# Kernel optimization log

Measured on AMD Instinct MI355X. Metric: run time of the kernel, lower is better.

Reference implementation:

```python
import jax, jax.numpy as jnp
from jax import lax
import numpy as np
import math

IMG_H, IMG_W = 592, 800  # stride-16 image for a 50x37 feature map


def _make_anchors(fx=50, fy=37, base=8, dsr=16):
    rows = []
    for x in range(fx):
        for y in range(fy):
            for size in [base, 2 * base, 4 * base]:
                rows.append([(x - size / 2) * dsr, (y - size / 2) * dsr,
                             (x + size / 2) * dsr, (y + size / 2) * dsr])
                s = math.sqrt(size ** 2 / 2)
                rows.append([(x - s) * dsr, (y - s / 2) * dsr, (x + s) * dsr, (y + s / 2) * dsr])
                rows.append([(x - s / 2) * dsr, (y - s) * dsr, (x + s / 2) * dsr, (y + s) * dsr])
    return np.array(rows, np.float32)


def setup_inputs() -> dict:
    key = jax.random.key(0)
    k = jax.random.split(key, 8)
    B, G, H, W = 32, 20, 50, 37
    feats = jax.random.normal(k[0], (B, 512, H, W), jnp.float32)
    a = _make_anchors()
    keep = (a[:, 0] >= 0) & (a[:, 1] >= 0) & (a[:, 2] <= IMG_W) & (a[:, 3] <= IMG_H)
    idxs_inside = jnp.asarray(np.nonzero(keep)[0].astype(np.int32))
    anchors = jnp.asarray(a[keep])
    # valid xyxy GT boxes inside the image
    x1 = jax.random.uniform(k[1], (B, G)) * (IMG_W - 160)
    y1 = jax.random.uniform(k[2], (B, G)) * (IMG_H - 160)
    w = 32.0 + jax.random.uniform(k[3], (B, G)) * 96.0
    h = 32.0 + jax.random.uniform(k[4], (B, G)) * 96.0
    gt_boxes = jnp.stack([x1, y1, x1 + w, y1 + h], -1)
    W3 = jax.random.normal(k[5], (512, 512, 3, 3), jnp.float32) * 0.02
    b3 = jnp.zeros((512,), jnp.float32)
    Wcls = jax.random.normal(k[6], (18, 512, 1, 1), jnp.float32) * 0.02
    bcls = jnp.zeros((18,), jnp.float32)
    Wloc = jax.random.normal(k[7], (36, 512, 1, 1), jnp.float32) * 0.02
    bloc = jnp.zeros((36,), jnp.float32)
    return {"feats": feats, "gt_boxes": gt_boxes, "anchors": anchors,
            "W3": W3, "b3": b3, "Wcls": Wcls, "bcls": bcls,
            "Wloc": Wloc, "bloc": bloc, "idxs_inside": idxs_inside}


def _conv(x, w, b, pad):
    y = lax.conv_general_dilated(x, w, (1, 1), pad,
                                 dimension_numbers=("NCHW", "OIHW", "NCHW"))
    return y + b[None, :, None, None]


def reference(feats, gt_boxes, anchors, W3, b3, Wcls, bcls, Wloc, bloc, idxs_inside):
    B = feats.shape[0]
    rpn_conv1 = jax.nn.relu(_conv(feats, W3, b3, "SAME"))
    cls_score = _conv(rpn_conv1, Wcls, bcls, "VALID")          # [B,18,H,W]
    _, C, H, Wd = cls_score.shape
    logits = cls_score.reshape(B, 2, (C * H) // 2, Wd)          # reshape(x, 2)
    prob = jax.nn.softmax(logits, axis=1)
    prob_back = prob.reshape(B, C, H, Wd)                       # reshape back to 18
    loc_pred = _conv(rpn_conv1, Wloc, bloc, "VALID")            # [B,36,H,W]

    # select inside-image anchors
    logits_sel = logits.transpose(0, 2, 3, 1).reshape(B, -1, 2)[:, idxs_inside, :]
    loc_sel = loc_pred.transpose(0, 2, 3, 1).reshape(B, -1, 4)[:, idxs_inside, :]

    # vectorized anchors x gt IoU (replaces the triple python loop)
    ix1 = jnp.maximum(anchors[None, :, None, 0], gt_boxes[:, None, :, 0])
    iy1 = jnp.maximum(anchors[None, :, None, 1], gt_boxes[:, None, :, 1])
    ix2 = jnp.minimum(anchors[None, :, None, 2], gt_boxes[:, None, :, 2])
    iy2 = jnp.minimum(anchors[None, :, None, 3], gt_boxes[:, None, :, 3])
    inter = jnp.clip(ix2 - ix1, 0) * jnp.clip(iy2 - iy1, 0)     # [B,A,G]
    area_a = (anchors[:, 2] - anchors[:, 0]) * (anchors[:, 3] - anchors[:, 1])
    area_g = (gt_boxes[..., 2] - gt_boxes[..., 0]) * (gt_boxes[..., 3] - gt_boxes[..., 1])
    iou = inter / jnp.maximum(area_a[None, :, None] + area_g[:, None, :] - inter, 1e-8)

    max_iou = iou.max(-1)                                       # [B,A]
    matched = iou.argmax(-1)                                    # [B,A] gt index per anchor
    gt_best = iou.argmax(1)                                     # [B,G] best anchor per gt
    A = anchors.shape[0]
    is_best = jnp.zeros((B, A), bool).at[jnp.arange(B)[:, None], gt_best].set(True)
    labels = (is_best | (max_iou > 0.7)).astype(jnp.int32)      # positives=1, rest 0

    logsm = jax.nn.log_softmax(logits_sel, -1)
    loss_cls = -jnp.take_along_axis(logsm, labels[..., None], -1).mean()

    tgt = jnp.take_along_axis(gt_boxes, matched[:, :, None], axis=1)  # [B,A,4]
    d = loc_sel - tgt
    sl1 = jnp.where(jnp.abs(d) < 1.0, 0.5 * d * d, jnp.abs(d) - 0.5)
    loss_loc = (sl1 * labels[..., None].astype(sl1.dtype)).sum() / 256.0

    return prob_back, loc_pred, loss_cls, loss_loc
```

## Files before the change

### kernel.cpp

```cpp
#include <hip/hip_runtime.h>
#include <stdint.h>

typedef unsigned short u16;
typedef unsigned int   u32;
typedef unsigned long long u64;

typedef __bf16 v8bf __attribute__((ext_vector_type(8)));
typedef float  v4f  __attribute__((ext_vector_type(4)));

#define NBATCH 32
#define NCH    512
#define FH     50
#define FW     37
#define PIX    1850
#define MTOT   59200
#define KTOT   4608
#define HP     52
#define WP     39
#define NG     20
#define W3N    (NCH*KTOT)
#define WCBN   (64*512)
#define BORDN  364544
#define NT     72

#define PROB_N 1065600
#define LC_IDX 3196800
#define LL_IDX 3196801

__device__ __forceinline__ u16 f2bf(float f) {
    u32 u = __float_as_uint(f);
    u += 0x7fffu + ((u >> 16) & 1u);
    return (u16)(u >> 16);
}

__device__ __forceinline__ void gl_lds16(const u16* g, u16* l) {
    __builtin_amdgcn_global_load_lds((const __attribute__((address_space(1))) u32*)g,
                                     (__attribute__((address_space(3))) u32*)l,
                                     16, 0, 0);
}

__device__ __forceinline__ int offA_of(int T, int kh) {
    const int dydx = T >> 3;
    const int ci0  = (T & 7) << 6;
    return ((dydx / 3) * WP + (dydx % 3)) * NCH + ci0 + kh * 32;
}

__global__ __launch_bounds__(256) void pad_kernel(const float* __restrict__ feats,
                                                  u16* __restrict__ fpad) {
    __shared__ float t[64][65];
    const int b  = blockIdx.z;
    const int c0 = blockIdx.y * 64;
    const int p0 = blockIdx.x * 64;
    const int tid = threadIdx.x;
    {
        const int cl = tid >> 2, seg = tid & 3;
        const float* src = feats + ((size_t)b * NCH + c0 + cl) * PIX;
        const int pbase = p0 + seg * 16;
        #pragma unroll
        for (int i = 0; i < 16; i++) {
            int p = pbase + i;
            t[cl][seg * 16 + i] = (p < PIX) ? src[p] : 0.f;
        }
    }
    __syncthreads();
    {
        const int pl = tid >> 2, cs = tid & 3;
        const int p = p0 + pl;
        if (p < PIX) {
            const int h = p / FW, w = p % FW;
            size_t dst = (((size_t)b * HP + h + 1) * WP + (w + 1)) * NCH + c0 + cs * 16;
            u32 pk[8];
            #pragma unroll
            for (int i = 0; i < 8; i++) {
                u32 lo = f2bf(t[cs * 16 + 2 * i][pl]);
                u32 hi = f2bf(t[cs * 16 + 2 * i + 1][pl]);
                pk[i] = lo | (hi << 16);
            }
            *(uint4*)&fpad[dst]     = make_uint4(pk[0], pk[1], pk[2], pk[3]);
            *(uint4*)&fpad[dst + 8] = make_uint4(pk[4], pk[5], pk[6], pk[7]);
        }
    }
}

__global__ void prep_kernel(const float* __restrict__ w3, const float* __restrict__ wcls,
                            const float* __restrict__ wloc,
                            u16* __restrict__ wbt, u16* __restrict__ wcb,
                            u16* __restrict__ fpad, float* __restrict__ out) {
    int t = blockIdx.x * 256 + threadIdx.x;
    if (t < 2) out[LC_IDX + t] = 0.f;
    if (t < W3N) {
        int co = t / KTOT, k = t % KTOT;
        int dydx = k >> 9, ci = k & 511;
        wbt[t] = f2bf(w3[((size_t)co * NCH + ci) * 9 + dydx]);
    } else if (t < W3N + WCBN) {
        int t2 = t - W3N;
        int c = t2 >> 9, ci = t2 & 511;
        float v = (c < 18) ? wcls[c * 512 + ci]
                : (c < 54) ? wloc[(c - 18) * 512 + ci] : 0.f;
        wcb[t2] = f2bf(v);
    } else if (t < W3N + WCBN + BORDN) {
        int t3 = t - (W3N + WCBN);
        int c8 = t3 & 63;
        int pi = (t3 >> 6) % 178;
        int b  = (t3 >> 6) / 178;
        int h, w;
        if (pi < 39)       { h = 0;        w = pi; }
        else if (pi < 78)  { h = 51;       w = pi - 39; }
        else if (pi < 128) { h = pi - 77;  w = 0; }
        else               { h = pi - 127; w = 38; }
        size_t dst = (((size_t)b * HP + h) * WP + w) * NCH + c8 * 8;
        *(uint4*)&fpad[dst] = make_uint4(0, 0, 0, 0);
    }
}

__global__ __launch_bounds__(512) void conv3x3_mfma(const u16* __restrict__ fpad,
                                                    const u16* __restrict__ wbt,
                                                    const float* __restrict__ b3,
                                                    u16* __restrict__ conv1) {
    __shared__ __align__(16) u16 As[2][2][256][32];
    __shared__ __align__(16) u16 Bs[2][2][256][32];

    const int wg     = ((int)blockIdx.x & 7) * 58 + ((int)blockIdx.x >> 3);
    const int n_base = (wg & 1) * 256;
    const int m_base = (wg >> 1) * 256;

    const int tid = threadIdx.x;
    const int w   = tid >> 6;
    const int l   = tid & 63;

    const int sr   = l >> 2;
    const int sseg = (l & 3) ^ ((l >> 3) & 3);
    int rbA[2], rbB[2];
    #pragma unroll
    for (int c = 0; c < 2; c++) {
        const int r  = w * 32 + c * 16 + sr;
        const int m  = m_base + r;
        const int mm = (m < MTOT) ? m : 0;
        const int b = mm / PIX, p = mm % PIX;
        const int y = p / FW, x = p % FW;
        rbA[c] = ((b * HP + y) * WP + x) * NCH + sseg * 8;
        rbB[c] = (n_base + r) * KTOT + sseg * 8;
    }
    u16* const aBase = &As[0][0][0][0] + w * 1024;
    u16* const bBase = &Bs[0][0][0][0] + w * 1024;

    const int wm = w >> 2, wn = w & 3;
    const int lm = l & 15, quad = l >> 4;
    const int psw = (quad ^ ((lm >> 1) & 3)) * 8;
    const u16* const aR = &As[0][0][0][0] + (wm * 128 + lm) * 32 + psw;
    const u16* const bR = &Bs[0][0][0][0] + (wn * 64  + lm) * 32 + psw;

    v4f acc[8][4];
    #pragma unroll
    for (int i = 0; i < 8; i++)
        #pragma unroll
        for (int j = 0; j < 4; j++)
            #pragma unroll
            for (int r = 0; r < 4; r++) acc[i][j][r] = 0.f;

    v8bf af[4], bfv[4];

#define STAGE_A(buf, kh, Tp) { \
        const int oA_ = offA_of((Tp), (kh)); \
        u16* const dA_ = aBase + (buf) * 16384 + (kh) * 8192; \
        gl_lds16(fpad + rbA[0] + oA_, dA_); \
        gl_lds16(fpad + rbA[1] + oA_, dA_ + 512); }
#define STAGE_B(buf, kh, Tp) { \
        const int oB_ = (Tp) * 64 + (kh) * 32; \
        u16* const dB_ = bBase + (buf) * 16384 + (kh) * 8192; \
        gl_lds16(wbt + rbB[0] + oB_, dB_); \
        gl_lds16(wbt + rbB[1] + oB_, dB_ + 512); }

    STAGE_A(0, 0, 0); STAGE_B(0, 0, 0);
    STAGE_A(0, 1, 0); STAGE_B(0, 1, 0);
    STAGE_A(1, 0, 1); STAGE_B(1, 0, 1);
    asm volatile("s_waitcnt vmcnt(4)" ::: "memory");
    __builtin_amdgcn_s_barrier();

#define PHASE(kh, mh, STAGE_STMT, TAIL_STMT) { \
        const int kof_ = cb * 16384 + (kh) * 8192; \
        if ((mh) == 0) { \
            _Pragma("unroll") \
            for (int nj = 0; nj < 4; nj++) \
                bfv[nj] = *(const v8bf*)(bR + kof_ + nj * 512); \
        } \
        _Pragma("unroll") \
        for (int i = 0; i < 4; i++) \
            af[i] = *(const v8bf*)(aR + kof_ + ((mh) * 4 + i) * 512); \
        STAGE_STMT; \
        __builtin_amdgcn_s_barrier(); \
        asm volatile("s_waitcnt lgkmcnt(0)"); \
        __builtin_amdgcn_sched_barrier(0); \
        __builtin_amdgcn_s_setprio(1); \
        _Pragma("unroll") \
        for (int i = 0; i < 4; i++) \
            _Pragma("unroll") \
            for (int nj = 0; nj < 4; nj++) \
                acc[(mh) * 4 + i][nj] = __builtin_amdgcn_mfma_f32_16x16x32_bf16( \
                    af[i], bfv[nj], acc[(mh) * 4 + i][nj], 0, 0, 0); \
        __builtin_amdgcn_s_setprio(0); \
        TAIL_STMT; \
        __builtin_amdgcn_s_barrier(); }

    for (int T = 0; T < NT; ++T) {
        const int cb = T & 1;
        const int nb = cb ^ 1;
        PHASE(0, 0, { if (T < NT - 1) STAGE_A(nb, 1, T + 1); }, {});
        PHASE(0, 1, { if (T < NT - 1) STAGE_B(nb, 1, T + 1); }, {});
        PHASE(1, 0, { if (T < NT - 2) STAGE_A(cb, 0, T + 2); }, {});
        PHASE(1, 1, { if (T < NT - 2) STAGE_B(cb, 0, T + 2); },
              { if (T < NT - 2)       { asm volatile("s_waitcnt vmcnt(4)" ::: "memory"); }
                else if (T == NT - 2) { asm volatile("s_waitcnt vmcnt(0)" ::: "memory"); } });
    }
#undef PHASE
#undef STAGE_A
#undef STAGE_B

    #pragma unroll
    for (int nj = 0; nj < 4; nj++) {
        const int n = n_base + wn * 64 + nj * 16 + lm;
        const float bias = b3[n];
        #pragma unroll
        for (int i = 0; i < 8; i++) {
            #pragma unroll
            for (int r = 0; r < 4; r++) {
                const int m = m_base + wm * 128 + i * 16 + quad * 4 + r;
                if (m < MTOT) {
                    float v = acc[i][nj][r] + bias;
                    v = v > 0.f ? v : 0.f;
                    conv1[(size_t)m * NCH + n] = f2bf(v);
                }
            }
        }
    }
}

__global__ __launch_bounds__(256) void head_mfma(const u16* __restrict__ conv1,
                                                 const u16* __restrict__ wcb,
                                                 const float* __restrict__ bcls,
                                                 const float* __restrict__ bloc,
                                                 float* __restrict__ out) {
    __shared__ __align__(16) u16 As[128][64];
    __shared__ __align__(16) u16 Bs[64][64];
    __shared__ float ct[128][66];

    const int tid = threadIdx.x;
    const int m_base = blockIdx.x * 128;
    const int wave = tid >> 6;
    const int lane = tid & 63;
    const int srow  = tid >> 3;
    const int seg_g = (tid & 7) ^ (srow & 7);

    int rbA[4];
    #pragma unroll
    for (int r = 0; r < 4; r++) {
        int m = m_base + r * 32 + srow;
        int mm = (m < MTOT) ? m : 0;
        rbA[r] = mm * NCH + seg_g * 8;
    }
    int rbB[2];
    #pragma unroll
    for (int r = 0; r < 2; r++)
        rbB[r] = (r * 32 + srow) * NCH + seg_g * 8;

    u16* const asb = &As[0][0] + wave * 512;
    u16* const bsb = &Bs[0][0] + wave * 512;

    const int wn = wave * 16;
    const int lm = lane & 15;
    const int quad = lane >> 4;
    const int x7 = lm & 7;

    v4f acc[8];
    #pragma unroll
    for (int i = 0; i < 8; i++)
        #pragma unroll
        for (int r = 0; r < 4; r++) acc[i][r] = 0.f;

    for (int k0 = 0; k0 < NCH; k0 += 64) {
        #pragma unroll
        for (int r = 0; r < 4; r++)
            gl_lds16(conv1 + rbA[r] + k0, asb + r * 2048);
        #pragma unroll
        for (int r = 0; r < 2; r++)
            gl_lds16(wcb + rbB[r] + k0, bsb + r * 2048);
        __syncthreads();

        #pragma unroll
        for (int kh = 0; kh < 2; kh++) {
            const int ps = (((kh << 2) | quad) ^ x7) * 8;
            v8bf bf = *(const v8bf*)(&Bs[0][0] + (wn + lm) * 64 + ps);
            #pragma unroll
            for (int i = 0; i < 8; i++) {
                v8bf af = *(const v8bf*)(&As[0][0] + (i * 16 + lm) * 64 + ps);
                acc[i] = __builtin_amdgcn_mfma_f32_16x16x32_bf16(af, bf, acc[i], 0, 0, 0);
            }
        }
        __syncthreads();
    }

    const int col = wn + lm;
    const float bias = (col < 18) ? bcls[col] : (col < 54) ? bloc[col - 18] : 0.f;
    #pragma unroll
    for (int i = 0; i < 8; i++)
        #pragma unroll
        for (int r = 0; r < 4; r++)
            ct[i * 16 + quad * 4 + r][col] = acc[i][r] + bias;
    __syncthreads();

    const int c = tid >> 2;
    const int pix4 = tid & 3;
    for (int px = pix4; px < 128; px += 4) {
        const int m = m_base + px;
        if (m >= MTOT) break;
        const int b = m / PIX;
        const int p = m - b * PIX;
        if (c < 9) {
            float s0 = ct[px][c], s1 = ct[px][c + 9];
            float mx = fmaxf(s0, s1);
            float e0 = __expf(s0 - mx), e1 = __expf(s1 - mx);
            float inv = 1.f / (e0 + e1);
            out[((size_t)b * 18 + c) * PIX + p]     = e0 * inv;
            out[((size_t)b * 18 + c + 9) * PIX + p] = e1 * inv;
        } else if (c >= 18 && c < 54) {
            out[(size_t)PROB_N + ((size_t)b * 36 + (c - 18)) * PIX + p] = ct[px][c];
        }
    }
}

__global__ __launch_bounds__(256) void iouloss_kernel(const float* __restrict__ anchors,
                                                      const float* __restrict__ gtb,
                                                      const int* __restrict__ idxs,
                                                      int A,
                                                      const float* __restrict__ outr,
                                                      float* __restrict__ out) {
    __shared__ float g[NG * 4];
    __shared__ u64 keys[NG];
    __shared__ int gbest[NG];
    __shared__ float red[8];
    const int b = blockIdx.y;
    const int tid = threadIdx.x;
    if (tid < NG * 4) g[tid] = gtb[b * NG * 4 + tid];
    if (tid < NG) keys[tid] = 0ull;
    __syncthreads();

    u64 lk[NG];
    #pragma unroll
    for (int gi = 0; gi < NG; gi++) lk[gi] = 0ull;
    for (int a = tid; a < A; a += 256) {
        const float ax1 = anchors[a * 4 + 0], ay1 = anchors[a * 4 + 1];
        const float ax2 = anchors[a * 4 + 2], ay2 = anchors[a * 4 + 3];
        const float areaA = (ax2 - ax1) * (ay2 - ay1);
        const u64 atag = (u64)(0xFFFFFFFFu - (u32)a);
        #pragma unroll
        for (int gi = 0; gi < NG; gi++) {
            float gx1 = g[gi*4], gy1 = g[gi*4+1], gx2 = g[gi*4+2], gy2 = g[gi*4+3];
            float iw = fmaxf(fminf(ax2, gx2) - fmaxf(ax1, gx1), 0.f);
            float ih = fmaxf(fminf(ay2, gy2) - fmaxf(ay1, gy1), 0.f);
            float inter = iw * ih;
            float areaG = (gx2 - gx1) * (gy2 - gy1);
            float iou = inter / fmaxf(areaA + areaG - inter, 1e-8f);
            u64 key = (((u64)__float_as_uint(iou)) << 32) | atag;
            if (key > lk[gi]) lk[gi] = key;
        }
    }
    #pragma unroll
    for (int gi = 0; gi < NG; gi++) {
        u64 k = lk[gi];
        #pragma unroll
        for (int off = 32; off; off >>= 1) {
            u64 o = __shfl_xor(k, off);
            k = (o > k) ? o : k;
        }
        if ((tid & 63) == 0) atomicMax(&keys[gi], k);
    }
    __syncthreads();
    if (tid < NG) gbest[tid] = (int)(0xFFFFFFFFu - (u32)(keys[tid] & 0xFFFFFFFFull));
    __syncthreads();

    float lc = 0.f, ll = 0.f;
    for (int a = tid; a < A; a += 256) {
        const float ax1 = anchors[a * 4 + 0], ay1 = anchors[a * 4 + 1];
        const float ax2 = anchors[a * 4 + 2], ay2 = anchors[a * 4 + 3];
        const float areaA = (ax2 - ax1) * (ay2 - ay1);
        float best = -1.f;
        int bg = 0;
        #pragma unroll
        for (int gi = 0; gi < NG; gi++) {
            float gx1 = g[gi*4], gy1 = g[gi*4+1], gx2 = g[gi*4+2], gy2 = g[gi*4+3];
            float iw = fmaxf(fminf(ax2, gx2) - fmaxf(ax1, gx1), 0.f);
            float ih = fmaxf(fminf(ay2, gy2) - fmaxf(ay1, gy1), 0.f);
            float inter = iw * ih;
            float areaG = (gx2 - gx1) * (gy2 - gy1);
            float iou = inter / fmaxf(areaA + areaG - inter, 1e-8f);
            if (iou > best) { best = iou; bg = gi; }
        }
        int lbl = (best > 0.7f) ? 1 : 0;
        if (!lbl) {
            #pragma unroll
            for (int gi = 0; gi < NG; gi++) lbl |= (gbest[gi] == a);
        }
        const int idx = idxs[a];
        const int cpr = idx / PIX;
        const int rem = idx % PIX;
        float p0 = outr[((size_t)b * 18 + cpr) * PIX + rem];
        float p1 = outr[((size_t)b * 18 + cpr + 9) * PIX + rem];
        lc += -logf(lbl ? p1 : p0);
        if (lbl) {
            const int hh = idx / 333;
            const int r2 = idx % 333;
            const int ww = r2 / 9;
            const int c4 = r2 % 9;
            const int pp = hh * FW + ww;
            #pragma unroll
            for (int t = 0; t < 4; t++) {
                float lv = outr[(size_t)PROB_N + ((size_t)b * 36 + c4 * 4 + t) * PIX + pp];
                float d = lv - g[bg * 4 + t];
                float ad = fabsf(d);
                ll += (ad < 1.f) ? 0.5f * d * d : ad - 0.5f;
            }
        }
    }
    #pragma unroll
    for (int off = 32; off; off >>= 1) {
        lc += __shfl_xor(lc, off);
        ll += __shfl_xor(ll, off);
    }
    const int lane = tid & 63, wave = tid >> 6;
    if (lane == 0) { red[wave] = lc; red[4 + wave] = ll; }
    __syncthreads();
    if (tid == 0) {
        float slc = red[0] + red[1] + red[2] + red[3];
        float sll = red[4] + red[5] + red[6] + red[7];
        atomicAdd(&out[LC_IDX], slc * (1.f / (32.f * (float)A)));
        atomicAdd(&out[LL_IDX], sll * (1.f / 256.f));
    }
}

extern "C" void kernel_launch(void* const* d_in, const int* in_sizes, int n_in,
                              void* d_out, int out_size, void* d_ws, size_t ws_size,
                              hipStream_t stream) {
    const float* feats   = (const float*)d_in[0];
    const float* gtb     = (const float*)d_in[1];
    const float* anchors = (const float*)d_in[2];
    const float* W3      = (const float*)d_in[3];
    const float* b3      = (const float*)d_in[4];
    const float* Wcls    = (const float*)d_in[5];
    const float* bcls    = (const float*)d_in[6];
    const float* Wloc    = (const float*)d_in[7];
    const float* bloc    = (const float*)d_in[8];
    const int*   idxs    = (const int*)d_in[9];
    const int A = in_sizes[9];
    float* out = (float*)d_out;

    char* ws = (char*)d_ws;
    size_t off = 0;
    auto alloc = [&](size_t bytes) -> void* {
        void* p = ws + off;
        off = (off + bytes + 255) & ~(size_t)255;
        return p;
    };
    const size_t fpad_n = (size_t)NBATCH * HP * WP * NCH;
    u16* fpad   = (u16*)alloc(fpad_n * 2);
    u16* wbt    = (u16*)alloc((size_t)W3N * 2);
    u16* wcb    = (u16*)alloc((size_t)WCBN * 2);
    u16* conv1  = (u16*)alloc((size_t)MTOT * NCH * 2);

    const int prep_tot = W3N + WCBN + BORDN;
    prep_kernel<<<(prep_tot + 255) / 256, 256, 0, stream>>>(W3, Wcls, Wloc, wbt, wcb, fpad, out);
    pad_kernel<<<dim3(29, 8, NBATCH), 256, 0, stream>>>(feats, fpad);
    conv3x3_mfma<<<464, 512, 0, stream>>>(fpad, wbt, b3, conv1);
    head_mfma<<<463, 256, 0, stream>>>(conv1, wcb, bcls, bloc, out);
    iouloss_kernel<<<dim3(1, NBATCH), 256, 0, stream>>>(anchors, gtb, idxs, A, out, out);
}
```

Before: 778.3 us.

## Double-buffer MFMA register fragments so LDS reads overlap matrix math

Restructures the conv3x3 main loop so each phase issues the LDS fragment reads for the next MFMA block before running the current one, using two sets of A and B register fragments (ping-pong). The explicit lgkmcnt wait and sched barrier before each MFMA group are removed, and the vmcnt thresholds and barrier placement are adjusted to the new staging order. Launch bounds now ask for 2 workgroups per CU. This is meant to hide LDS latency behind MFMA, at the cost of more VGPRs (a pressure risk under the occupancy hint) and a more delicate barrier/waitcnt ordering.

```diff
diff --git a/kernel.cpp b/kernel.cpp
--- a/kernel.cpp
+++ b/kernel.cpp
@@ -113,10 +113,10 @@
     }
 }
 
-__global__ __launch_bounds__(512) void conv3x3_mfma(const u16* __restrict__ fpad,
-                                                    const u16* __restrict__ wbt,
-                                                    const float* __restrict__ b3,
-                                                    u16* __restrict__ conv1) {
+__global__ __launch_bounds__(512, 2) void conv3x3_mfma(const u16* __restrict__ fpad,
+                                                       const u16* __restrict__ wbt,
+                                                       const float* __restrict__ b3,
+                                                       u16* __restrict__ conv1) {
     __shared__ __align__(16) u16 As[2][2][256][32];
     __shared__ __align__(16) u16 Bs[2][2][256][32];
 
@@ -158,7 +158,7 @@
             #pragma unroll
             for (int r = 0; r < 4; r++) acc[i][j][r] = 0.f;
 
-    v8bf af[4], bfv[4];
+    v8bf afA[4], afB[4], bf0[4], bf1[4];
 
 #define STAGE_A(buf, kh, Tp) { \
         const int oA_ = offA_of((Tp), (kh)); \
@@ -170,51 +170,66 @@
         u16* const dB_ = bBase + (buf) * 16384 + (kh) * 8192; \
         gl_lds16(wbt + rbB[0] + oB_, dB_); \
         gl_lds16(wbt + rbB[1] + oB_, dB_ + 512); }
+#define RD_A(dst, buf, kh, mh) { \
+        _Pragma("unroll") \
+        for (int i_ = 0; i_ < 4; i_++) \
+            dst[i_] = *(const v8bf*)(aR + (buf) * 16384 + (kh) * 8192 + ((mh) * 4 + i_) * 512); }
+#define RD_B(dst, buf, kh) { \
+        _Pragma("unroll") \
+        for (int j_ = 0; j_ < 4; j_++) \
+            dst[j_] = *(const v8bf*)(bR + (buf) * 16384 + (kh) * 8192 + j_ * 512); }
+#define MM(afv, bfv, mh) { \
+        __builtin_amdgcn_s_setprio(1); \
+        _Pragma("unroll") \
+        for (int i_ = 0; i_ < 4; i_++) \
+            _Pragma("unroll") \
+            for (int j_ = 0; j_ < 4; j_++) \
+                acc[(mh) * 4 + i_][j_] = __builtin_amdgcn_mfma_f32_16x16x32_bf16( \
+                    afv[i_], bfv[j_], acc[(mh) * 4 + i_][j_], 0, 0, 0); \
+        __builtin_amdgcn_s_setprio(0); }
 
     STAGE_A(0, 0, 0); STAGE_B(0, 0, 0);
     STAGE_A(0, 1, 0); STAGE_B(0, 1, 0);
     STAGE_A(1, 0, 1); STAGE_B(1, 0, 1);
     asm volatile("s_waitcnt vmcnt(4)" ::: "memory");
     __builtin_amdgcn_s_barrier();
-
-#define PHASE(kh, mh, STAGE_STMT, TAIL_STMT) { \
-        const int kof_ = cb * 16384 + (kh) * 8192; \
-        if ((mh) == 0) { \
-            _Pragma("unroll") \
-            for (int nj = 0; nj < 4; nj++) \
-                bfv[nj] = *(const v8bf*)(bR + kof_ + nj * 512); \
-        } \
-        _Pragma("unroll") \
-        for (int i = 0; i < 4; i++) \
-            af[i] = *(const v8bf*)(aR + kof_ + ((mh) * 4 + i) * 512); \
-        STAGE_STMT; \
-        __builtin_amdgcn_s_barrier(); \
-        asm volatile("s_waitcnt lgkmcnt(0)"); \
-        __builtin_amdgcn_sched_barrier(0); \
-        __builtin_amdgcn_s_setprio(1); \
-        _Pragma("unroll") \
-        for (int i = 0; i < 4; i++) \
-            _Pragma("unroll") \
-            for (int nj = 0; nj < 4; nj++) \
-                acc[(mh) * 4 + i][nj] = __builtin_amdgcn_mfma_f32_16x16x32_bf16( \
-                    af[i], bfv[nj], acc[(mh) * 4 + i][nj], 0, 0, 0); \
-        __builtin_amdgcn_s_setprio(0); \
-        TAIL_STMT; \
-        __builtin_amdgcn_s_barrier(); }
+    RD_A(afA, 0, 0, 0); RD_B(bf0, 0, 0);
 
     for (int T = 0; T < NT; ++T) {
         const int cb = T & 1;
         const int nb = cb ^ 1;
-        PHASE(0, 0, { if (T < NT - 1) STAGE_A(nb, 1, T + 1); }, {});
-        PHASE(0, 1, { if (T < NT - 1) STAGE_B(nb, 1, T + 1); }, {});
-        PHASE(1, 0, { if (T < NT - 2) STAGE_A(cb, 0, T + 2); }, {});
-        PHASE(1, 1, { if (T < NT - 2) STAGE_B(cb, 0, T + 2); },
-              { if (T < NT - 2)       { asm volatile("s_waitcnt vmcnt(4)" ::: "memory"); }
-                else if (T == NT - 2) { asm volatile("s_waitcnt vmcnt(0)" ::: "memory"); } });
-    }
-#undef PHASE
+        RD_A(afB, cb, 0, 1);
+        if (T + 1 < NT) STAGE_A(nb, 1, T + 1);
+        __builtin_amdgcn_s_barrier();
+        MM(afA, bf0, 0);
+        if (T < NT - 1) { asm volatile("s_waitcnt vmcnt(6)" ::: "memory"); }
+        else            { asm volatile("s_waitcnt vmcnt(0)" ::: "memory"); }
+        __builtin_amdgcn_s_barrier();
+        RD_A(afA, cb, 1, 0);
+        RD_B(bf1, cb, 1);
+        if (T + 1 < NT) STAGE_B(nb, 1, T + 1);
+        __builtin_amdgcn_s_barrier();
+        MM(afB, bf0, 1);
+        __builtin_amdgcn_s_barrier();
+        RD_A(afB, cb, 1, 1);
+        if (T + 2 < NT) STAGE_A(cb, 0, T + 2);
+        __builtin_amdgcn_s_barrier();
+        MM(afA, bf1, 0);
+        if (T < NT - 2)       { asm volatile("s_waitcnt vmcnt(6)" ::: "memory"); }
+        else if (T == NT - 2) { asm volatile("s_waitcnt vmcnt(4)" ::: "memory"); }
+        else                  { asm volatile("s_waitcnt vmcnt(0)" ::: "memory"); }
+        __builtin_amdgcn_s_barrier();
+        if (T + 1 < NT) { RD_A(afA, nb, 0, 0); RD_B(bf0, nb, 0); }
+        if (T + 2 < NT) STAGE_B(cb, 0, T + 2);
+        __builtin_amdgcn_s_barrier();
+        MM(afB, bf1, 1);
+        __builtin_amdgcn_s_barrier();
+    }
+#undef MM
+#undef RD_B
+#undef RD_A
+#undef STAGE_B
 #undef STAGE_A
-#undef STAGE_B
 
     #pragma unroll
     for (int nj = 0; nj < 4; nj++) {
```

After: 781.3 us. No clear change (+0.4%).
